# Optimization experiments

Measured on AMD Instinct MI355X. Metric: run time of the kernel, lower is better.

The kernel has to match this reference:

```python
import jax, jax.numpy as jnp
import numpy as np

B, IN, OUT, HS, NBDA = 128, 256, 256, 512, 1

def setup_inputs() -> dict:
    key = jax.random.key(0)
    ks = jax.random.split(key, 16)
    d = {}
    d["inputs"] = jax.random.normal(ks[0], (B, IN), dtype=jnp.float32)
    d["hidden"] = jax.random.normal(ks[1], (B, HS), dtype=jnp.float32)
    d["hebb"] = jax.random.normal(ks[2], (B, HS, HS), dtype=jnp.float32) * 0.1
    # learned params (torch.nn.Linear: y = x @ W.T + b)
    d["i2h_w"] = jax.random.normal(ks[3], (HS, IN), dtype=jnp.float32) * (1.0 / np.sqrt(IN))
    d["i2h_b"] = jnp.zeros((HS,), dtype=jnp.float32)
    d["w"] = 0.01 * jax.random.uniform(ks[4], (HS, HS), dtype=jnp.float32)
    d["alpha"] = 0.01 * jax.random.uniform(ks[5], (HS, HS), dtype=jnp.float32)
    d["h2o_w"] = jax.random.normal(ks[6], (OUT, HS), dtype=jnp.float32) * (1.0 / np.sqrt(HS))
    d["h2o_b"] = jnp.zeros((OUT,), dtype=jnp.float32)
    d["h2v_w"] = jax.random.normal(ks[7], (1, HS), dtype=jnp.float32) * (1.0 / np.sqrt(HS))
    d["h2v_b"] = jnp.zeros((1,), dtype=jnp.float32)
    d["h2da_w"] = jax.random.normal(ks[8], (NBDA, HS), dtype=jnp.float32) * (1.0 / np.sqrt(HS))
    d["h2da_b"] = jnp.zeros((NBDA,), dtype=jnp.float32)
    return d

def reference(inputs, hidden, hebb, i2h_w, i2h_b, w, alpha, h2o_w, h2o_b,
              h2v_w, h2v_b, h2da_w, h2da_b):
    # hactiv = tanh(i2h(x) + (w + alpha*hebb) @ hidden), per-sample weight matrix
    pre = inputs @ i2h_w.T + i2h_b                              # [B, HS]
    w_eff = w + alpha * hebb                                    # [B, HS, HS]
    rec = jnp.einsum('bij,bj->bi', w_eff, hidden)               # [B, HS]
    hactiv = jnp.tanh(pre + rec)                                # [B, HS]
    activout = hactiv @ h2o_w.T + h2o_b                         # [B, OUT]
    valueout = hactiv @ h2v_w.T + h2v_b                         # [B, 1]
    da = jnp.tanh(hactiv @ h2da_w.T + h2da_b)                   # [B, NBDA]
    # outer-product Hebbian update, DA-modulated, clamped to [-1, 1]
    deltahebb = hactiv[:, :, None] * hidden[:, None, :]         # [B, HS, HS]
    hebb_new = jnp.clip(hebb + da[:, :1, None] * deltahebb, -1.0, 1.0)
    return activout, valueout, hactiv, hebb_new
```

## Files before the change

kernel.cpp:

```cpp
#include <hip/hip_runtime.h>
#include <cstddef>
#include <cstdint>

#define B_    128
#define IN_   256
#define OUT_  256
#define HS_   512

#define NTHR_  512
#define NBLK_  512
#define SPLIT_ 4

__device__ __forceinline__ float clip1(float x) {
    return fminf(fmaxf(x, -1.f), 1.f);
}

__global__ __launch_bounds__(NTHR_, 2) void fused_stream(
    const float* __restrict__ inputs,
    const float* __restrict__ hidden,
    const float* __restrict__ hebb,
    const float* __restrict__ i2h_w,
    const float* __restrict__ i2h_b,
    const float* __restrict__ w,
    const float* __restrict__ alpha,
    const float* __restrict__ h2o_w,
    const float* __restrict__ h2o_b,
    const float* __restrict__ h2v_w,
    const float* __restrict__ h2v_b,
    const float* __restrict__ h2da_w,
    const float* __restrict__ h2da_b,
    float* __restrict__ activout,
    float* __restrict__ valueout,
    float* __restrict__ hactiv,
    float* __restrict__ hebb_new,
    float* __restrict__ ws_pd,
    float* __restrict__ ws_pv,
    int*   __restrict__ ws_cnt)
{
    const int blk  = blockIdx.x;
    const int xcd  = blk & 7;
    const int g    = blk >> 3;
    const int q16  = g >> 2;
    const int s    = g & 3;
    const int b    = xcd * 16 + q16;
    const int tid  = threadIdx.x;
    const int wave = tid >> 6;
    const int lane = tid & 63;
    const int r0   = s * 128 + wave * 16;
    const int lr0  = wave * 16;

    __shared__ float s_hrow[128];
    __shared__ float s_pd[8], s_pv[8];
    __shared__ float s_bc[2];
    __shared__ float s_h[HS_];
    __shared__ float s_part[256];

    const float4* hid4 = (const float4*)(hidden + (size_t)b * HS_);
    const float4 h0  = hid4[lane];
    const float4 h1  = hid4[lane + 64];
    const float4 in4 = ((const float4*)(inputs + (size_t)b * IN_))[lane];

    const float4* hb4 = (const float4*)hebb + ((size_t)b * HS_) * (HS_ / 4);
    const float4* w4  = (const float4*)w;
    const float4* a4  = (const float4*)alpha;
    const float4* iw4 = (const float4*)i2h_w;

    float pd = 0.f, pv = 0.f;
    for (int t = 0; t < 16; t += 2) {
        const int i = r0 + t;
        const float4* hpA = hb4 + (size_t)i * (HS_ / 4);
        const float4* hpB = hpA + (HS_ / 4);
        const float4* wpA = w4  + (size_t)i * (HS_ / 4);
        const float4* apA = a4  + (size_t)i * (HS_ / 4);
        const float4* ipA = iw4 + (size_t)i * (IN_ / 4);

        const float4 xA0 = hpA[lane],            xA1 = hpA[lane + 64];
        const float4 xB0 = hpB[lane],            xB1 = hpB[lane + 64];
        const float4 wA0 = wpA[lane],            wA1 = wpA[lane + 64];
        const float4 wB0 = wpA[128 + lane],      wB1 = wpA[128 + lane + 64];
        const float4 aA0 = apA[lane],            aA1 = apA[lane + 64];
        const float4 aB0 = apA[128 + lane],      aB1 = apA[128 + lane + 64];
        const float4 iA  = ipA[lane];
        const float4 iB  = ipA[64 + lane];

        float a, c;
        a  = (wA0.x + aA0.x * xA0.x) * h0.x;
        a += (wA0.y + aA0.y * xA0.y) * h0.y;
        a += (wA0.z + aA0.z * xA0.z) * h0.z;
        a += (wA0.w + aA0.w * xA0.w) * h0.w;
        a += (wA1.x + aA1.x * xA1.x) * h1.x;
        a += (wA1.y + aA1.y * xA1.y) * h1.y;
        a += (wA1.z + aA1.z * xA1.z) * h1.z;
        a += (wA1.w + aA1.w * xA1.w) * h1.w;
        a += iA.x * in4.x + iA.y * in4.y + iA.z * in4.z + iA.w * in4.w;

        c  = (wB0.x + aB0.x * xB0.x) * h0.x;
        c += (wB0.y + aB0.y * xB0.y) * h0.y;
        c += (wB0.z + aB0.z * xB0.z) * h0.z;
        c += (wB0.w + aB0.w * xB0.w) * h0.w;
        c += (wB1.x + aB1.x * xB1.x) * h1.x;
        c += (wB1.y + aB1.y * xB1.y) * h1.y;
        c += (wB1.z + aB1.z * xB1.z) * h1.z;
        c += (wB1.w + aB1.w * xB1.w) * h1.w;
        c += iB.x * in4.x + iB.y * in4.y + iB.z * in4.z + iB.w * in4.w;

        #pragma unroll
        for (int off = 1; off < 64; off <<= 1) {
            a += __shfl_xor(a, off, 64);
            c += __shfl_xor(c, off, 64);
        }

        const float hA = tanhf(a + i2h_b[i]);
        const float hB = tanhf(c + i2h_b[i + 1]);
        if (lane == 0) {
            s_hrow[lr0 + t]     = hA;
            s_hrow[lr0 + t + 1] = hB;
            float2* hp = (float2*)(hactiv + (size_t)b * HS_ + i);
            *hp = make_float2(hA, hB);
            pd += hA * h2da_w[i] + hB * h2da_w[i + 1];
            pv += hA * h2v_w[i]  + hB * h2v_w[i + 1];
        }
    }

    if (lane == 0) { s_pd[wave] = pd; s_pv[wave] = pv; }
    __syncthreads();

    if (tid == 0) {
        float sd = 0.f, sv = 0.f;
        #pragma unroll
        for (int k = 0; k < 8; ++k) { sd += s_pd[k]; sv += s_pv[k]; }
        __hip_atomic_fetch_add(&ws_pd[b], sd, __ATOMIC_RELAXED,
                               __HIP_MEMORY_SCOPE_AGENT);
        __hip_atomic_fetch_add(&ws_pv[b], sv, __ATOMIC_RELAXED,
                               __HIP_MEMORY_SCOPE_AGENT);
        __hip_atomic_fetch_add(&ws_cnt[b], 1, __ATOMIC_RELEASE,
                               __HIP_MEMORY_SCOPE_AGENT);
        while (__hip_atomic_load(&ws_cnt[b], __ATOMIC_ACQUIRE,
                                 __HIP_MEMORY_SCOPE_AGENT) < SPLIT_)
            __builtin_amdgcn_s_sleep(1);
        const float pdt = __hip_atomic_load(&ws_pd[b], __ATOMIC_RELAXED,
                                            __HIP_MEMORY_SCOPE_AGENT);
        const float pvt = __hip_atomic_load(&ws_pv[b], __ATOMIC_RELAXED,
                                            __HIP_MEMORY_SCOPE_AGENT);
        s_bc[0] = tanhf(pdt + h2da_b[0]);
        s_bc[1] = pvt + h2v_b[0];
    }
    __syncthreads();
    const float da_b = s_bc[0];
    if (s == 0 && tid == 0)
        valueout[b] = s_bc[1];

    for (int t = 0; t < 16; t += 2) {
        const int i = r0 + t;
        const float4* xp = hb4 + (size_t)i * (HS_ / 4);
        const float4 x0 = xp[lane],       x1 = xp[lane + 64];
        const float4 y0 = xp[128 + lane], y1 = xp[128 + lane + 64];
        const float scA = da_b * s_hrow[lr0 + t];
        const float scB = da_b * s_hrow[lr0 + t + 1];

        float4 o0, o1, p0, p1;
        o0.x = clip1(fmaf(scA, h0.x, x0.x));
        o0.y = clip1(fmaf(scA, h0.y, x0.y));
        o0.z = clip1(fmaf(scA, h0.z, x0.z));
        o0.w = clip1(fmaf(scA, h0.w, x0.w));
        o1.x = clip1(fmaf(scA, h1.x, x1.x));
        o1.y = clip1(fmaf(scA, h1.y, x1.y));
        o1.z = clip1(fmaf(scA, h1.z, x1.z));
        o1.w = clip1(fmaf(scA, h1.w, x1.w));
        p0.x = clip1(fmaf(scB, h0.x, y0.x));
        p0.y = clip1(fmaf(scB, h0.y, y0.y));
        p0.z = clip1(fmaf(scB, h0.z, y0.z));
        p0.w = clip1(fmaf(scB, h0.w, y0.w));
        p1.x = clip1(fmaf(scB, h1.x, y1.x));
        p1.y = clip1(fmaf(scB, h1.y, y1.y));
        p1.z = clip1(fmaf(scB, h1.z, y1.z));
        p1.w = clip1(fmaf(scB, h1.w, y1.w));

        float4* dp = (float4*)hebb_new + ((size_t)b * HS_ + i) * (HS_ / 4);
        dp[lane]            = o0;
        dp[lane + 64]       = o1;
        dp[128 + lane]      = p0;
        dp[128 + lane + 64] = p1;
    }

    if (tid < 128)
        ((float4*)s_h)[tid] = ((const float4*)(hactiv + (size_t)b * HS_))[tid];
    __syncthreads();

    if (tid < 256) {
        const int ol = tid & 63;
        const int qq = tid >> 6;
        const int o  = s * 64 + ol;
        const float4* wp  = (const float4*)(h2o_w + (size_t)o * HS_);
        const float4* hp4 = (const float4*)s_h;
        float acc = 0.f;
        #pragma unroll
        for (int c2 = 0; c2 < 32; ++c2) {
            const float4 wv = wp[qq * 32 + c2];
            const float4 hv = hp4[qq * 32 + c2];
            acc += wv.x * hv.x + wv.y * hv.y + wv.z * hv.z + wv.w * hv.w;
        }
        s_part[qq * 64 + ol] = acc;
    }
    __syncthreads();
    if (tid < 64) {
        const int o = s * 64 + tid;
        activout[(size_t)b * OUT_ + o] =
            s_part[tid] + s_part[64 + tid] + s_part[128 + tid] +
            s_part[192 + tid] + h2o_b[o];
    }
}

__global__ __launch_bounds__(256) void k1_hactiv(
    const float* __restrict__ inputs, const float* __restrict__ hidden,
    const float* __restrict__ hebb, const float* __restrict__ i2h_w,
    const float* __restrict__ i2h_b, const float* __restrict__ w,
    const float* __restrict__ alpha, float* __restrict__ hactiv)
{
    const int b     = blockIdx.x & (B_ - 1);
    const int chunk = blockIdx.x >> 7;
    const int tid   = threadIdx.x;
    const int wave  = tid >> 6;
    const int lane  = tid & 63;

    const float4* hid4 = (const float4*)(hidden + (size_t)b * HS_);
    const float4  h0   = hid4[lane];
    const float4  h1   = hid4[lane + 64];
    const float4  in4  = ((const float4*)(inputs + (size_t)b * IN_))[lane];

    const int i0 = chunk * 64 + wave * 16;

    for (int r = 0; r < 16; ++r) {
        const int i = i0 + r;
        const float4* hb = (const float4*)(hebb + ((size_t)b * HS_ + i) * HS_);
        const float4* wr = (const float4*)(w     + (size_t)i * HS_);
        const float4* ar = (const float4*)(alpha + (size_t)i * HS_);

        const float4 hb0 = hb[lane];
        const float4 hb1 = hb[lane + 64];
        const float4 wv0 = wr[lane];
        const float4 wv1 = wr[lane + 64];
        const float4 av0 = ar[lane];
        const float4 av1 = ar[lane + 64];
        const float4 iw  = ((const float4*)(i2h_w + (size_t)i * IN_))[lane];

        float acc;
        acc  = (wv0.x + av0.x * hb0.x) * h0.x;
        acc += (wv0.y + av0.y * hb0.y) * h0.y;
        acc += (wv0.z + av0.z * hb0.z) * h0.z;
        acc += (wv0.w + av0.w * hb0.w) * h0.w;
        acc += (wv1.x + av1.x * hb1.x) * h1.x;
        acc += (wv1.y + av1.y * hb1.y) * h1.y;
        acc += (wv1.z + av1.z * hb1.z) * h1.z;
        acc += (wv1.w + av1.w * hb1.w) * h1.w;
        acc += iw.x * in4.x + iw.y * in4.y + iw.z * in4.z + iw.w * in4.w;

        #pragma unroll
        for (int off = 32; off > 0; off >>= 1)
            acc += __shfl_down(acc, off, 64);

        if (lane == 0)
            hactiv[(size_t)b * HS_ + i] = tanhf(acc + i2h_b[i]);
    }
}

__global__ __launch_bounds__(256) void k2_heads(
    const float* __restrict__ hactiv, const float* __restrict__ h2o_w,
    const float* __restrict__ h2o_b, const float* __restrict__ h2v_w,
    const float* __restrict__ h2v_b, const float* __restrict__ h2da_w,
    const float* __restrict__ h2da_b, float* __restrict__ activout,
    float* __restrict__ valueout, float* __restrict__ da)
{
    const int b   = blockIdx.x;
    const int tid = threadIdx.x;

    __shared__ float s_h[HS_];
    __shared__ float red_v[256];
    __shared__ float red_d[256];

    for (int t = tid; t < HS_; t += 256)
        s_h[t] = hactiv[(size_t)b * HS_ + t];
    __syncthreads();

    const float4* wr  = (const float4*)(h2o_w + (size_t)tid * HS_);
    const float4* sh4 = (const float4*)s_h;
    float acc = 0.f;
    #pragma unroll 4
    for (int q = 0; q < HS_ / 4; ++q) {
        const float4 wv = wr[q];
        const float4 hv = sh4[q];
        acc += wv.x * hv.x + wv.y * hv.y + wv.z * hv.z + wv.w * hv.w;
    }
    activout[(size_t)b * OUT_ + tid] = acc + h2o_b[tid];

    float pv = 0.f, pd = 0.f;
    for (int t = tid; t < HS_; t += 256) {
        const float hv = s_h[t];
        pv += hv * h2v_w[t];
        pd += hv * h2da_w[t];
    }
    red_v[tid] = pv;
    red_d[tid] = pd;
    __syncthreads();
    for (int s2 = 128; s2 > 0; s2 >>= 1) {
        if (tid < s2) {
            red_v[tid] += red_v[tid + s2];
            red_d[tid] += red_d[tid + s2];
        }
        __syncthreads();
    }
    if (tid == 0) {
        valueout[b] = red_v[0] + h2v_b[0];
        da[b]       = tanhf(red_d[0] + h2da_b[0]);
    }
}

__global__ __launch_bounds__(256) void k3_hebb(
    const float* __restrict__ hebb, const float* __restrict__ hidden,
    const float* __restrict__ hactiv, const float* __restrict__ da,
    float* __restrict__ hebb_new)
{
    const int tid = threadIdx.x;
    const size_t base = (size_t)blockIdx.x * 1024;

    #pragma unroll
    for (int k = 0; k < 4; ++k) {
        const size_t idx = base + (size_t)k * 256 + tid;
        const int j4  = (int)(idx & 127);
        const int row = (int)(idx >> 7);
        const int i   = row & (HS_ - 1);
        const int b   = row >> 9;

        const float scale = da[b] * hactiv[(size_t)b * HS_ + i];
        const float4 hv = ((const float4*)hebb)[idx];
        const float4 hd = ((const float4*)hidden)[(size_t)b * (HS_ / 4) + j4];

        float4 r;
        r.x = fminf(fmaxf(fmaf(scale, hd.x, hv.x), -1.f), 1.f);
        r.y = fminf(fmaxf(fmaf(scale, hd.y, hv.y), -1.f), 1.f);
        r.z = fminf(fmaxf(fmaf(scale, hd.z, hv.z), -1.f), 1.f);
        r.w = fminf(fmaxf(fmaf(scale, hd.w, hv.w), -1.f), 1.f);
        ((float4*)hebb_new)[idx] = r;
    }
}

extern "C" void kernel_launch(void* const* d_in, const int* in_sizes, int n_in,
                              void* d_out, int out_size, void* d_ws, size_t ws_size,
                              hipStream_t stream)
{
    const float* inputs = (const float*)d_in[0];
    const float* hidden = (const float*)d_in[1];
    const float* hebb   = (const float*)d_in[2];
    const float* i2h_w  = (const float*)d_in[3];
    const float* i2h_b  = (const float*)d_in[4];
    const float* w      = (const float*)d_in[5];
    const float* alpha  = (const float*)d_in[6];
    const float* h2o_w  = (const float*)d_in[7];
    const float* h2o_b  = (const float*)d_in[8];
    const float* h2v_w  = (const float*)d_in[9];
    const float* h2v_b  = (const float*)d_in[10];
    const float* h2da_w = (const float*)d_in[11];
    const float* h2da_b = (const float*)d_in[12];

    float* out = (float*)d_out;
    float* activout = out;
    float* valueout = out + 32768;
    float* hactiv   = out + 32768 + 128;
    float* hebb_new = out + 32768 + 128 + 65536;

    const size_t gate_bytes = (size_t)(3 * B_) * sizeof(float);

    if (ws_size >= gate_bytes) {
        float* ws_pd  = (float*)d_ws;
        float* ws_pv  = ws_pd + B_;
        int*   ws_cnt = (int*)(ws_pv + B_);

        hipMemsetAsync(d_ws, 0, gate_bytes, stream);

        fused_stream<<<dim3(NBLK_), dim3(NTHR_), 0, stream>>>(
            inputs, hidden, hebb, i2h_w, i2h_b, w, alpha,
            h2o_w, h2o_b, h2v_w, h2v_b, h2da_w, h2da_b,
            activout, valueout, hactiv, hebb_new,
            ws_pd, ws_pv, ws_cnt);
    } else {
        float* da = (float*)d_ws;
        k1_hactiv<<<dim3(1024), dim3(256), 0, stream>>>(
            inputs, hidden, hebb, i2h_w, i2h_b, w, alpha, hactiv);
        k2_heads<<<dim3(B_), dim3(256), 0, stream>>>(
            hactiv, h2o_w, h2o_b, h2v_w, h2v_b, h2da_w, h2da_b,
            activout, valueout, da);
        k3_hebb<<<dim3(8192), dim3(256), 0, stream>>>(
            hebb, hidden, hactiv, da, hebb_new);
    }
}
```

Baseline: 327.4 us.

## Split each batch row across eight blocks and raise occupancy to four blocks

```diff
diff --git a/kernel.cpp b/kernel.cpp
--- a/kernel.cpp
+++ b/kernel.cpp
@@ -8,14 +8,14 @@
 #define HS_   512
 
 #define NTHR_  512
-#define NBLK_  512
-#define SPLIT_ 4
+#define NBLK_  1024
+#define SPLIT_ 8
 
 __device__ __forceinline__ float clip1(float x) {
     return fminf(fmaxf(x, -1.f), 1.f);
 }
 
-__global__ __launch_bounds__(NTHR_, 2) void fused_stream(
+__global__ __launch_bounds__(NTHR_, 4) void fused_stream(
     const float* __restrict__ inputs,
     const float* __restrict__ hidden,
     const float* __restrict__ hebb,
@@ -38,22 +38,19 @@
     int*   __restrict__ ws_cnt)
 {
     const int blk  = blockIdx.x;
-    const int xcd  = blk & 7;
-    const int g    = blk >> 3;
-    const int q16  = g >> 2;
-    const int s    = g & 3;
-    const int b    = xcd * 16 + q16;
+    const int b    = blk >> 3;
+    const int s    = blk & 7;
     const int tid  = threadIdx.x;
     const int wave = tid >> 6;
     const int lane = tid & 63;
-    const int r0   = s * 128 + wave * 16;
-    const int lr0  = wave * 16;
-
-    __shared__ float s_hrow[128];
+    const int r0   = s * 64 + wave * 8;
+    const int lr0  = wave * 8;
+
+    __shared__ float s_hrow[64];
     __shared__ float s_pd[8], s_pv[8];
     __shared__ float s_bc[2];
     __shared__ float s_h[HS_];
-    __shared__ float s_part[256];
+    __shared__ float s_part[512];
 
     const float4* hid4 = (const float4*)(hidden + (size_t)b * HS_);
     const float4 h0  = hid4[lane];
@@ -66,7 +63,7 @@
     const float4* iw4 = (const float4*)i2h_w;
 
     float pd = 0.f, pv = 0.f;
-    for (int t = 0; t < 16; t += 2) {
+    for (int t = 0; t < 8; t += 2) {
         const int i = r0 + t;
         const float4* hpA = hb4 + (size_t)i * (HS_ / 4);
         const float4* hpB = hpA + (HS_ / 4);
@@ -150,7 +147,7 @@
     if (s == 0 && tid == 0)
         valueout[b] = s_bc[1];
 
-    for (int t = 0; t < 16; t += 2) {
+    for (int t = 0; t < 8; t += 2) {
         const int i = r0 + t;
         const float4* xp = hb4 + (size_t)i * (HS_ / 4);
         const float4 x0 = xp[lane],       x1 = xp[lane + 64];
@@ -187,27 +184,29 @@
         ((float4*)s_h)[tid] = ((const float4*)(hactiv + (size_t)b * HS_))[tid];
     __syncthreads();
 
-    if (tid < 256) {
-        const int ol = tid & 63;
-        const int qq = tid >> 6;
-        const int o  = s * 64 + ol;
+    {
+        const int ol = tid & 31;
+        const int sg = tid >> 5;
+        const int o  = s * 32 + ol;
         const float4* wp  = (const float4*)(h2o_w + (size_t)o * HS_);
         const float4* hp4 = (const float4*)s_h;
         float acc = 0.f;
         #pragma unroll
-        for (int c2 = 0; c2 < 32; ++c2) {
-            const float4 wv = wp[qq * 32 + c2];
-            const float4 hv = hp4[qq * 32 + c2];
+        for (int c2 = 0; c2 < 8; ++c2) {
+            const float4 wv = wp[sg * 8 + c2];
+            const float4 hv = hp4[sg * 8 + c2];
             acc += wv.x * hv.x + wv.y * hv.y + wv.z * hv.z + wv.w * hv.w;
         }
-        s_part[qq * 64 + ol] = acc;
-    }
-    __syncthreads();
-    if (tid < 64) {
-        const int o = s * 64 + tid;
-        activout[(size_t)b * OUT_ + o] =
-            s_part[tid] + s_part[64 + tid] + s_part[128 + tid] +
-            s_part[192 + tid] + h2o_b[o];
+        s_part[sg * 32 + ol] = acc;
+    }
+    __syncthreads();
+    if (tid < 32) {
+        const int o = s * 32 + tid;
+        float acc = h2o_b[o];
+        #pragma unroll
+        for (int k = 0; k < 16; ++k)
+            acc += s_part[k * 32 + tid];
+        activout[(size_t)b * OUT_ + o] = acc;
     }
 }
 
@@ -370,7 +369,11 @@
 
     const size_t gate_bytes = (size_t)(3 * B_) * sizeof(float);
 
-    if (ws_size >= gate_bytes) {
+    int maxb = 0;
+    hipError_t oe = hipOccupancyMaxActiveBlocksPerMultiprocessor(
+        &maxb, fused_stream, NTHR_, 0);
+
+    if (ws_size >= gate_bytes && oe == hipSuccess && maxb >= 4) {
         float* ws_pd  = (float*)d_ws;
         float* ws_pv  = ws_pd + B_;
         int*   ws_cnt = (int*)(ws_pv + B_);
```

Measured after the change: 299.7 us. 1.09x faster.
